# Kernel tuning notes

Hardware: AMD Instinct MI355X
Metric: run time of the kernel (lower is better)

Reference implementation:

```python
import jax, jax.numpy as jnp
import numpy as np

B, S, E, H, F, V = 4, 2048, 1024, 16, 4096, 32000
D = E // H  # head_dim = 64
LN_EPS = 1e-5


def layer_norm(x, g, b):
    mu = jnp.mean(x, axis=-1, keepdims=True)
    var = jnp.mean(jnp.square(x - mu), axis=-1, keepdims=True)
    return (x - mu) * jax.lax.rsqrt(var + LN_EPS) * g + b


def setup_inputs() -> dict:
    key = jax.random.key(0)
    ks = jax.random.split(key, 12)
    s = 0.02
    return {
        "input_ids": jax.random.randint(ks[0], (B, S), 0, V),
        "attention_mask": jnp.ones((B, S), dtype=jnp.int32),
        "emb_table": jax.random.normal(ks[1], (V, E), jnp.float32) * s,
        "Wq": jax.random.normal(ks[2], (E, E), jnp.float32) * s,
        "bq": jnp.zeros((E,), jnp.float32),
        "Wk": jax.random.normal(ks[3], (E, E), jnp.float32) * s,
        "bk": jnp.zeros((E,), jnp.float32),
        "Wv": jax.random.normal(ks[4], (E, E), jnp.float32) * s,
        "bv": jnp.zeros((E,), jnp.float32),
        "Wo": jax.random.normal(ks[5], (E, E), jnp.float32) * s,
        "bo": jnp.zeros((E,), jnp.float32),
        "ln_g": jnp.ones((E,), jnp.float32),
        "ln_b": jnp.zeros((E,), jnp.float32),
        "W1": jax.random.normal(ks[6], (E, F), jnp.float32) * s,
        "b1": jnp.zeros((F,), jnp.float32),
        "W2": jax.random.normal(ks[7], (F, E), jnp.float32) * s,
        "b2": jnp.zeros((E,), jnp.float32),
        "Wp": jax.random.normal(ks[8], (E, 3), jnp.float32) * s,
        "bp": jnp.zeros((3,), jnp.float32),
    }


def reference(input_ids, attention_mask, emb_table, Wq, bq, Wk, bk, Wv, bv,
              Wo, bo, ln_g, ln_b, W1, b1, W2, b2, Wp, bp):
    b, s = input_ids.shape
    x = emb_table[input_ids]                                  # [B,S,E]
    q = (x @ Wq + bq).reshape(b, s, H, D).transpose(0, 2, 1, 3)  # [B,H,S,D]
    k = (x @ Wk + bk).reshape(b, s, H, D).transpose(0, 2, 1, 3)
    v = (x @ Wv + bv).reshape(b, s, H, D).transpose(0, 2, 1, 3)
    scores = jnp.einsum('bhqd,bhkd->bhqk', q, k) / jnp.sqrt(jnp.float32(D))
    mask = attention_mask[:, None, None, :]                   # [B,1,1,S]
    scores = jnp.where(mask == 0, -jnp.inf, scores)
    attn = jax.nn.softmax(scores, axis=-1)
    ctx = jnp.einsum('bhqk,bhkd->bhqd', attn, v)              # [B,H,S,D]
    ctx = ctx.transpose(0, 2, 1, 3).reshape(b, s, E)
    ctx = ctx @ Wo + bo
    h = layer_norm(ctx + x, ln_g, ln_b)
    ff = jax.nn.gelu(h @ W1 + b1, approximate=False) @ W2 + b2
    logits = ff @ Wp + bp                                     # [B,S,3]
    return logits.mean(axis=1)                                # [B,3]
```

## Files before the change

kernel.cpp:

```cpp
#include <hip/hip_runtime.h>
#include <hip/hip_bf16.h>
#include <math.h>

#define BB 4
#define SS 2048
#define EE 1024
#define HH 16
#define DD 64
#define FF 4096

typedef unsigned short u16;
typedef unsigned int u32;
typedef __bf16 bf16x8 __attribute__((ext_vector_type(8)));
typedef float f32x4 __attribute__((ext_vector_type(4)));

static __device__ __forceinline__ float gelu_exact(float v){
  return 0.5f * v * (1.0f + erff(v * 0.70710678118654752f));
}

static __device__ __forceinline__ u16 f2bf(float f){
  union { float f; u32 u; } x; x.f = f;
  u32 r = x.u + 0x7FFFu + ((x.u >> 16) & 1u);
  return (u16)(r >> 16);
}
static __device__ __forceinline__ void unpack2(u32 u, float& lo, float& hi){
  union { u32 u; float f; } a, b;
  a.u = u << 16; b.u = u & 0xFFFF0000u;
  lo = a.f; hi = b.f;
}

#define GLOAD_LDS16(g, l) \
  __builtin_amdgcn_global_load_lds((const __attribute__((address_space(1))) void*)(g), \
      (__attribute__((address_space(3))) void*)(l), 16, 0, 0)

__global__ __launch_bounds__(256) void embed_kernel(const int* __restrict__ ids,
    const float* __restrict__ emb, float* __restrict__ xf, u16* __restrict__ xbf){
  int row = blockIdx.x;
  int id  = ids[row];
  float4 v = ((const float4*)(emb + (size_t)id * EE))[threadIdx.x];
  ((float4*)(xf + (size_t)row * EE))[threadIdx.x] = v;
  ushort4 u; u.x = f2bf(v.x); u.y = f2bf(v.y); u.z = f2bf(v.z); u.w = f2bf(v.w);
  ((ushort4*)(xbf + (size_t)row * EE))[threadIdx.x] = u;
}

__global__ __launch_bounds__(256) void prep_weights(const float* __restrict__ Wq,
    const float* __restrict__ Wk, const float* __restrict__ Wv,
    const float* __restrict__ Wo, const float* __restrict__ W1, u16* __restrict__ WT){
  __shared__ float tile[32][33];
  int bid = blockIdx.x;
  const float* W; u16* dst; int N, n0, k0;
  if (bid < 4096){
    W = W1; dst = WT + (size_t)4 * EE * EE; N = FF;
    n0 = (bid & 127) * 32; k0 = (bid >> 7) * 32;
  } else {
    int idx = bid - 4096;
    int which = idx >> 10, t = idx & 1023;
    W = (which == 0) ? Wq : (which == 1) ? Wk : (which == 2) ? Wv : Wo;
    dst = WT + (size_t)which * EE * EE; N = EE;
    n0 = (t & 31) * 32; k0 = (t >> 5) * 32;
  }
  int tx = threadIdx.x & 31, ty = threadIdx.x >> 5;
  #pragma unroll
  for (int i = 0; i < 4; i++)
    tile[ty + 8*i][tx] = W[(size_t)(k0 + ty + 8*i) * N + n0 + tx];
  __syncthreads();
  #pragma unroll
  for (int i = 0; i < 4; i++)
    dst[(size_t)(n0 + ty + 8*i) * EE + k0 + tx] = f2bf(tile[tx][ty + 8*i]);
}

template<int MODE>
__global__ __launch_bounds__(256) void gemm_mfma(const u16* __restrict__ A,
    const u16* __restrict__ WT, const float* __restrict__ bias,
    const float* __restrict__ biasB, const float* __restrict__ biasC,
    u16* __restrict__ C, float* __restrict__ gsum, int M, int N, int K){
  __shared__ __attribute__((aligned(16))) u16 As[128 * 32];
  __shared__ __attribute__((aligned(16))) u16 Bs[128 * 32];

  const int tid = threadIdx.x;
  const int l = tid & 63, w = tid >> 6;
  const int lm = l & 15, lq = l >> 4;
  const int wm = (w >> 1) * 64, wn = (w & 1) * 64;
  const int r0 = blockIdx.y * 128, c0 = blockIdx.x * 128;

  const int srow0 = w * 32 + (l >> 2);
  const int scol  = (l & 3) * 8;
  const u16* Ab = A  + (size_t)(r0 + srow0) * K + scol;
  const u16* Bb = WT + (size_t)(c0 + srow0) * K + scol;
  u16* AsBase0 = &As[(w * 2)     * 512];
  u16* AsBase1 = &As[(w * 2 + 1) * 512];
  u16* BsBase0 = &Bs[(w * 2)     * 512];
  u16* BsBase1 = &Bs[(w * 2 + 1) * 512];

  f32x4 acc[4][4];
  const f32x4 zero = {0.f, 0.f, 0.f, 0.f};
  #pragma unroll
  for (int mi = 0; mi < 4; mi++)
    #pragma unroll
    for (int ni = 0; ni < 4; ni++) acc[mi][ni] = zero;

  for (int k0 = 0; k0 < K; k0 += 32){
    GLOAD_LDS16(Ab + k0,                    AsBase0);
    GLOAD_LDS16(Ab + (size_t)16 * K + k0,   AsBase1);
    GLOAD_LDS16(Bb + k0,                    BsBase0);
    GLOAD_LDS16(Bb + (size_t)16 * K + k0,   BsBase1);
    __syncthreads();

    bf16x8 af[4], bf[4];
    #pragma unroll
    for (int mi = 0; mi < 4; mi++)
      af[mi] = *(const bf16x8*)&As[(wm + mi*16 + lm) * 32 + lq * 8];
    #pragma unroll
    for (int ni = 0; ni < 4; ni++)
      bf[ni] = *(const bf16x8*)&Bs[(wn + ni*16 + lm) * 32 + lq * 8];
    #pragma unroll
    for (int mi = 0; mi < 4; mi++)
      #pragma unroll
      for (int ni = 0; ni < 4; ni++)
        acc[mi][ni] = __builtin_amdgcn_mfma_f32_16x16x32_bf16(af[mi], bf[ni], acc[mi][ni], 0, 0, 0);
    __syncthreads();
  }

  if constexpr (MODE == 0){
    #pragma unroll
    for (int ni = 0; ni < 4; ni++){
      int col = c0 + wn + ni*16 + lm;
      float bcol = bias[col];
      #pragma unroll
      for (int mi = 0; mi < 4; mi++){
        #pragma unroll
        for (int r = 0; r < 4; r++){
          int row = r0 + wm + mi*16 + lq*4 + r;
          C[(size_t)row * N + col] = f2bf(acc[mi][ni][r] + bcol);
        }
      }
    }
  } else if constexpr (MODE == 2){
    #pragma unroll
    for (int ni = 0; ni < 4; ni++){
      int col3 = c0 + wn + ni*16 + lm;
      int sel  = col3 >> 10;
      int colm = col3 & 1023;
      const float* bp_ = (sel == 0) ? bias : ((sel == 1) ? biasB : biasC);
      float bcol = bp_[colm];
      u16* dst = C + (size_t)sel * ((size_t)M * N);
      #pragma unroll
      for (int mi = 0; mi < 4; mi++){
        #pragma unroll
        for (int r = 0; r < 4; r++){
          int row = r0 + wm + mi*16 + lq*4 + r;
          dst[(size_t)row * N + colm] = f2bf(acc[mi][ni][r] + bcol);
        }
      }
    }
  } else {
    const int batch = r0 >> 11;
    #pragma unroll
    for (int ni = 0; ni < 4; ni++){
      int col = c0 + wn + ni*16 + lm;
      float bcol = bias[col];
      float cs = 0.f;
      #pragma unroll
      for (int mi = 0; mi < 4; mi++)
        #pragma unroll
        for (int r = 0; r < 4; r++)
          cs += gelu_exact(acc[mi][ni][r] + bcol);
      cs += __shfl_xor(cs, 16, 64);
      cs += __shfl_xor(cs, 32, 64);
      if (lq == 0) atomicAdd(&gsum[(size_t)batch * N + col], cs);
    }
  }
}

__global__ __launch_bounds__(256, 4) void attn_mfma(const u16* __restrict__ q,
    const u16* __restrict__ k, const u16* __restrict__ v,
    const int* __restrict__ mask, u16* __restrict__ ctx){
  const int bh = blockIdx.y, b = bh >> 4, h = bh & 15;
  const int q0 = blockIdx.x * 128;
  const int tid = threadIdx.x;
  const int w = tid >> 6, l = tid & 63, lm = l & 15, lq = l >> 4;

  __shared__ __attribute__((aligned(16))) u16 Kt[64 * 72];
  __shared__ __attribute__((aligned(16))) u16 Vt[64 * 72];
  __shared__ __attribute__((aligned(16))) u16 Pw[4][32 * 72];
  __shared__ float mb[64];

  bf16x8 aq[2][2];
  #pragma unroll
  for (int mg = 0; mg < 2; mg++){
    const u16* qrow = q + (size_t)(b*SS + q0 + w*32 + mg*16 + lm) * EE + h*DD + lq*8;
    aq[mg][0] = *(const bf16x8*)qrow;
    aq[mg][1] = *(const bf16x8*)(qrow + 32);
  }

  f32x4 occ[2][4];
  const f32x4 zero = {0.f,0.f,0.f,0.f};
  #pragma unroll
  for (int mg = 0; mg < 2; mg++)
    #pragma unroll
    for (int ni = 0; ni < 4; ni++) occ[mg][ni] = zero;
  float l_part[2][4] = {{0.f,0.f,0.f,0.f},{0.f,0.f,0.f,0.f}};

  const int kkey = tid >> 2, kc16 = (tid & 3) * 16;
  const u16* kbase = k + (size_t)(b*SS + kkey) * EE + h*DD + kc16;
  const int kp = tid & 31, vd0 = (tid >> 5) * 8;
  const u16* vbase0 = v + (size_t)(b*SS + 2*kp) * EE + h*DD + vd0;
  const u16* vbase1 = vbase0 + EE;

  uint4 kr0 = *(const uint4*)(kbase);
  uint4 kr1 = *(const uint4*)(kbase + 8);
  uint4 vr0 = *(const uint4*)(vbase0);
  uint4 vr1 = *(const uint4*)(vbase1);
  float mreg = 0.f;
  if (tid < 64) mreg = (mask[b*SS + tid] != 0) ? 0.f : -1e30f;

  const float SCALE_LOG2E = 0.125f * 1.4426950408889634f;

  for (int t0 = 0; t0 < SS; t0 += 64){
    *(uint4*)&Kt[kkey*72 + kc16]     = kr0;
    *(uint4*)&Kt[kkey*72 + kc16 + 8] = kr1;
    {
      union { uint4 u; u16 s[8]; } va, vb;
      va.u = vr0; vb.u = vr1;
      #pragma unroll
      for (int i = 0; i < 8; i++){
        u32 pk = (u32)va.s[i] | ((u32)vb.s[i] << 16);
        *(u32*)&Vt[(vd0 + i)*72 + 2*kp] = pk;
      }
    }
    if (tid < 64) mb[tid] = mreg;
    __syncthreads();

    if (t0 + 64 < SS){
      kr0 = *(const uint4*)(kbase + (size_t)(t0 + 64) * EE);
      kr1 = *(const uint4*)(kbase + (size_t)(t0 + 64) * EE + 8);
      vr0 = *(const uint4*)(vbase0 + (size_t)(t0 + 64) * EE);
      vr1 = *(const uint4*)(vbase1 + (size_t)(t0 + 64) * EE);
      if (tid < 64) mreg = (mask[b*SS + t0 + 64 + tid] != 0) ? 0.f : -1e30f;
    }

    #pragma unroll
    for (int mg = 0; mg < 2; mg++){
      #pragma unroll
      for (int ni = 0; ni < 4; ni++){
        bf16x8 b0 = *(const bf16x8*)&Kt[(ni*16 + lm)*72 + lq*8];
        bf16x8 b1 = *(const bf16x8*)&Kt[(ni*16 + lm)*72 + 32 + lq*8];
        f32x4 sc = zero;
        sc = __builtin_amdgcn_mfma_f32_16x16x32_bf16(aq[mg][0], b0, sc, 0, 0, 0);
        sc = __builtin_amdgcn_mfma_f32_16x16x32_bf16(aq[mg][1], b1, sc, 0, 0, 0);
        float mbias = mb[ni*16 + lm];
        #pragma unroll
        for (int r = 0; r < 4; r++){
          float s = fminf(fmaf(sc[r], SCALE_LOG2E, mbias), 80.f);
          float p = __builtin_amdgcn_exp2f(s);
          l_part[mg][r] += p;
          Pw[w][(mg*16 + lq*4 + r)*72 + ni*16 + lm] = f2bf(p);
        }
      }
    }
    bf16x8 ap[2][2];
    #pragma unroll
    for (int mg = 0; mg < 2; mg++){
      ap[mg][0] = *(const bf16x8*)&Pw[w][(mg*16 + lm)*72 + lq*8];
      ap[mg][1] = *(const bf16x8*)&Pw[w][(mg*16 + lm)*72 + 32 + lq*8];
    }

    #pragma unroll
    for (int ni = 0; ni < 4; ni++){
      bf16x8 vb0 = *(const bf16x8*)&Vt[(ni*16 + lm)*72 + lq*8];
      bf16x8 vb1 = *(const bf16x8*)&Vt[(ni*16 + lm)*72 + 32 + lq*8];
      #pragma unroll
      for (int mg = 0; mg < 2; mg++){
        occ[mg][ni] = __builtin_amdgcn_mfma_f32_16x16x32_bf16(ap[mg][0], vb0, occ[mg][ni], 0, 0, 0);
        occ[mg][ni] = __builtin_amdgcn_mfma_f32_16x16x32_bf16(ap[mg][1], vb1, occ[mg][ni], 0, 0, 0);
      }
    }
    __syncthreads();
  }

  #pragma unroll
  for (int mg = 0; mg < 2; mg++){
    float inv[4];
    #pragma unroll
    for (int r = 0; r < 4; r++){
      float s = l_part[mg][r];
      s += __shfl_xor(s, 1, 64);
      s += __shfl_xor(s, 2, 64);
      s += __shfl_xor(s, 4, 64);
      s += __shfl_xor(s, 8, 64);
      inv[r] = 1.f / s;
    }
    #pragma unroll
    for (int ni = 0; ni < 4; ni++){
      int col = h*DD + ni*16 + lm;
      #pragma unroll
      for (int r = 0; r < 4; r++){
        int row = q0 + w*32 + mg*16 + lq*4 + r;
        ctx[(size_t)(b*SS + row) * EE + col] = f2bf(occ[mg][ni][r] * inv[r]);
      }
    }
  }
}

__global__ __launch_bounds__(256) void ln_kernel(const u16* __restrict__ c2,
    const float* __restrict__ x, const float* __restrict__ g,
    const float* __restrict__ bta, u16* __restrict__ h){
  int row = blockIdx.x, tid = threadIdx.x;
  uint2 cu = ((const uint2*)(c2 + (size_t)row * EE))[tid];
  float c0,c1,c2f,c3;
  unpack2(cu.x, c0, c1); unpack2(cu.y, c2f, c3);
  float4 xv = ((const float4*)(x + (size_t)row * EE))[tid];
  float4 y = make_float4(c0+xv.x, c1+xv.y, c2f+xv.z, c3+xv.w);
  float s  = y.x + y.y + y.z + y.w;
  float ss = y.x*y.x + y.y*y.y + y.z*y.z + y.w*y.w;
  #pragma unroll
  for (int off=32; off; off>>=1){
    s  += __shfl_xor(s,  off, 64);
    ss += __shfl_xor(ss, off, 64);
  }
  __shared__ float rs[4], rss[4];
  int w = tid >> 6;
  if ((tid & 63) == 0){ rs[w] = s; rss[w] = ss; }
  __syncthreads();
  float tot  = rs[0]+rs[1]+rs[2]+rs[3];
  float tots = rss[0]+rss[1]+rss[2]+rss[3];
  float mu  = tot  * (1.f/EE);
  float var = tots * (1.f/EE) - mu*mu;
  float inv = rsqrtf(var + 1e-5f);
  float4 gv = ((const float4*)g)[tid];
  float4 bv = ((const float4*)bta)[tid];
  ushort4 ou;
  ou.x = f2bf((y.x-mu)*inv*gv.x + bv.x);
  ou.y = f2bf((y.y-mu)*inv*gv.y + bv.y);
  ou.z = f2bf((y.z-mu)*inv*gv.z + bv.z);
  ou.w = f2bf((y.w-mu)*inv*gv.w + bv.w);
  ((ushort4*)(h + (size_t)row * EE))[tid] = ou;
}

__global__ __launch_bounds__(256) void w2wp_kernel(const float* __restrict__ W2,
    const float* __restrict__ Wp, float* __restrict__ W2Wp){
  int f0 = blockIdx.x * 8;
  int tid = threadIdx.x;
  int e0 = tid * 4;
  float wp[4][3];
  #pragma unroll
  for (int t = 0; t < 4; t++)
    #pragma unroll
    for (int j = 0; j < 3; j++) wp[t][j] = Wp[(e0 + t)*3 + j];
  __shared__ float red[3][4];
  for (int i = 0; i < 8; i++){
    int f = f0 + i;
    float4 wv = ((const float4*)(W2 + (size_t)f * EE))[tid];
    float w4[4] = {wv.x, wv.y, wv.z, wv.w};
    float p[3] = {0.f, 0.f, 0.f};
    #pragma unroll
    for (int t = 0; t < 4; t++)
      #pragma unroll
      for (int j = 0; j < 3; j++) p[j] += w4[t] * wp[t][j];
    #pragma unroll
    for (int j = 0; j < 3; j++){
      float sj = p[j];
      #pragma unroll
      for (int off = 32; off; off >>= 1) sj += __shfl_xor(sj, off, 64);
      if ((tid & 63) == 0) red[j][tid >> 6] = sj;
    }
    __syncthreads();
    if (tid < 3) W2Wp[f*3 + tid] = red[tid][0] + red[tid][1] + red[tid][2] + red[tid][3];
    __syncthreads();
  }
}

__global__ __launch_bounds__(256) void out_final(const float* __restrict__ gsum,
    const float* __restrict__ W2Wp, const float* __restrict__ b2,
    const float* __restrict__ Wp, const float* __restrict__ bp, float* __restrict__ out){
  int tid = threadIdx.x;
  float part[4][3];
  #pragma unroll
  for (int b = 0; b < 4; b++)
    #pragma unroll
    for (int j = 0; j < 3; j++) part[b][j] = 0.f;
  for (int f = tid; f < FF; f += 256){
    float w0 = W2Wp[f*3], w1 = W2Wp[f*3+1], w2v = W2Wp[f*3+2];
    #pragma unroll
    for (int b = 0; b < 4; b++){
      float g = gsum[b*FF + f] * (1.f/SS);
      part[b][0] += g * w0; part[b][1] += g * w1; part[b][2] += g * w2v;
    }
  }
  float bb[3] = {0.f, 0.f, 0.f};
  for (int e = tid; e < EE; e += 256){
    float bv = b2[e];
    bb[0] += bv * Wp[e*3]; bb[1] += bv * Wp[e*3+1]; bb[2] += bv * Wp[e*3+2];
  }
  __shared__ float red[15][4];
  int lane = tid & 63, w = tid >> 6;
  #pragma unroll
  for (int b = 0; b < 4; b++)
    #pragma unroll
    for (int j = 0; j < 3; j++){
      float s = part[b][j];
      #pragma unroll
      for (int off = 32; off; off >>= 1) s += __shfl_xor(s, off, 64);
      if (lane == 0) red[b*3 + j][w] = s;
    }
  #pragma unroll
  for (int j = 0; j < 3; j++){
    float s = bb[j];
    #pragma unroll
    for (int off = 32; off; off >>= 1) s += __shfl_xor(s, off, 64);
    if (lane == 0) red[12 + j][w] = s;
  }
  __syncthreads();
  if (tid < 12){
    int j = tid % 3;
    float s  = red[tid][0] + red[tid][1] + red[tid][2] + red[tid][3];
    float bj = red[12+j][0] + red[12+j][1] + red[12+j][2] + red[12+j][3];
    out[tid] = s + bj + bp[j];
  }
}

extern "C" void kernel_launch(void* const* d_in, const int* in_sizes, int n_in,
                              void* d_out, int out_size, void* d_ws, size_t ws_size,
                              hipStream_t stream) {
  const int M = BB * SS;
  const int* ids  = (const int*)d_in[0];
  const int* mask = (const int*)d_in[1];
  const float* emb = (const float*)d_in[2];
  const float* Wq = (const float*)d_in[3];  const float* bq = (const float*)d_in[4];
  const float* Wk = (const float*)d_in[5];  const float* bk = (const float*)d_in[6];
  const float* Wv = (const float*)d_in[7];  const float* bv = (const float*)d_in[8];
  const float* Wo = (const float*)d_in[9];  const float* bo = (const float*)d_in[10];
  const float* lg = (const float*)d_in[11]; const float* lb = (const float*)d_in[12];
  const float* W1 = (const float*)d_in[13]; const float* b1 = (const float*)d_in[14];
  const float* W2 = (const float*)d_in[15]; const float* b2 = (const float*)d_in[16];
  const float* Wp = (const float*)d_in[17]; const float* bp = (const float*)d_in[18];

  char* base = (char*)d_ws;
  const size_t SLOTF = (size_t)M * EE;
  float* xf   = (float*)base;
  u16*  xbf   = (u16*)(base + SLOTF*4);
  u16*  qbf   = (u16*)(base + SLOTF*6);
  u16*  kbf   = (u16*)(base + SLOTF*8);
  u16*  vbf   = (u16*)(base + SLOTF*10);
  u16*  ctxbf = (u16*)(base + SLOTF*12);
  u16*  c2bf  = qbf;
  u16*  hbf   = kbf;
  u16*  WqT   = (u16*)(base + SLOTF*14);
  u16*  W1T   = WqT + (size_t)4*EE*EE;
  float* gsum = (float*)(W1T + (size_t)FF*EE);
  float* w2wp = gsum + BB*FF;

  hipMemsetAsync(gsum, 0, BB*FF*sizeof(float), stream);

  embed_kernel<<<M, 256, 0, stream>>>(ids, emb, xf, xbf);

  prep_weights<<<8192, 256, 0, stream>>>(Wq, Wk, Wv, Wo, W1, WqT);
  w2wp_kernel<<<FF/8, 256, 0, stream>>>(W2, Wp, w2wp);

  gemm_mfma<2><<<dim3(3*EE/128, M/128), 256, 0, stream>>>(
      xbf, WqT, bq, bk, bv, qbf, nullptr, M, EE, EE);

  attn_mfma<<<dim3(SS/128, BB*HH), 256, 0, stream>>>(qbf, kbf, vbf, mask, ctxbf);

  gemm_mfma<0><<<dim3(EE/128, M/128), 256, 0, stream>>>(
      ctxbf, WqT + (size_t)3*EE*EE, bo, nullptr, nullptr, c2bf, nullptr, M, EE, EE);

  ln_kernel<<<M, 256, 0, stream>>>(c2bf, xf, lg, lb, hbf);

  gemm_mfma<1><<<dim3(FF/128, M/128), 256, 0, stream>>>(
      hbf, W1T, b1, nullptr, nullptr, nullptr, gsum, M, FF, EE);

  out_final<<<1, 256, 0, stream>>>(gsum, w2wp, b2, Wp, bp, (float*)d_out);
}
```

Measured before the change: 614.9 us.

## Keep attention probabilities in registers via transposed MFMA and lane shuffles

The attention kernel now computes the transposed score tile (K as the A operand, Q as B), so each lane holds probabilities laid out along the key dimension. The values are then repacked into the B-operand layout of the PV MFMA with cross-lane shuffles, which removes the per-wave shared-memory P buffer and its scalar stores and reloads. The output is likewise transposed, so row sums need only two shuffles and the context is written as 8-byte vector stores. In exchange it adds shuffle and select instructions and some register pressure, and the operand-layout changes must be exactly right to stay correct.

```diff
diff --git a/kernel.cpp b/kernel.cpp
--- a/kernel.cpp
+++ b/kernel.cpp
@@ -182,8 +182,7 @@
 
   __shared__ __attribute__((aligned(16))) u16 Kt[64 * 72];
   __shared__ __attribute__((aligned(16))) u16 Vt[64 * 72];
-  __shared__ __attribute__((aligned(16))) u16 Pw[4][32 * 72];
-  __shared__ float mb[64];
+  __shared__ __attribute__((aligned(16))) float mb[64];
 
   bf16x8 aq[2][2];
   #pragma unroll
@@ -198,8 +197,8 @@
   #pragma unroll
   for (int mg = 0; mg < 2; mg++)
     #pragma unroll
-    for (int ni = 0; ni < 4; ni++) occ[mg][ni] = zero;
-  float l_part[2][4] = {{0.f,0.f,0.f,0.f},{0.f,0.f,0.f,0.f}};
+    for (int mi = 0; mi < 4; mi++) occ[mg][mi] = zero;
+  float l_part[2] = {0.f, 0.f};
 
   const int kkey = tid >> 2, kc16 = (tid & 3) * 16;
   const u16* kbase = k + (size_t)(b*SS + kkey) * EE + h*DD + kc16;
@@ -239,40 +238,61 @@
       if (tid < 64) mreg = (mask[b*SS + t0 + 64 + tid] != 0) ? 0.f : -1e30f;
     }
 
+    bf16x8 pb[2][2];
     #pragma unroll
     for (int mg = 0; mg < 2; mg++){
-      #pragma unroll
-      for (int ni = 0; ni < 4; ni++){
-        bf16x8 b0 = *(const bf16x8*)&Kt[(ni*16 + lm)*72 + lq*8];
-        bf16x8 b1 = *(const bf16x8*)&Kt[(ni*16 + lm)*72 + 32 + lq*8];
-        f32x4 sc = zero;
-        sc = __builtin_amdgcn_mfma_f32_16x16x32_bf16(aq[mg][0], b0, sc, 0, 0, 0);
-        sc = __builtin_amdgcn_mfma_f32_16x16x32_bf16(aq[mg][1], b1, sc, 0, 0, 0);
-        float mbias = mb[ni*16 + lm];
+      float lp = 0.f;
+      #pragma unroll
+      for (int h2 = 0; h2 < 2; h2++){
+        u32 pk[2][2];
         #pragma unroll
-        for (int r = 0; r < 4; r++){
-          float s = fminf(fmaf(sc[r], SCALE_LOG2E, mbias), 80.f);
-          float p = __builtin_amdgcn_exp2f(s);
-          l_part[mg][r] += p;
-          Pw[w][(mg*16 + lq*4 + r)*72 + ni*16 + lm] = f2bf(p);
+        for (int np = 0; np < 2; np++){
+          int ni = h2*2 + np;
+          bf16x8 kf0 = *(const bf16x8*)&Kt[(ni*16 + lm)*72 + lq*8];
+          bf16x8 kf1 = *(const bf16x8*)&Kt[(ni*16 + lm)*72 + 32 + lq*8];
+          f32x4 sc = zero;
+          sc = __builtin_amdgcn_mfma_f32_16x16x32_bf16(kf0, aq[mg][0], sc, 0, 0, 0);
+          sc = __builtin_amdgcn_mfma_f32_16x16x32_bf16(kf1, aq[mg][1], sc, 0, 0, 0);
+          f32x4 mbv = *(const f32x4*)&mb[ni*16 + lq*4];
+          float p[4];
+          #pragma unroll
+          for (int r = 0; r < 4; r++){
+            float s = fminf(fmaf(sc[r], SCALE_LOG2E, mbv[r]), 80.f);
+            p[r] = __builtin_amdgcn_exp2f(s);
+            lp += p[r];
+          }
+          pk[np][0] = (u32)f2bf(p[0]) | ((u32)f2bf(p[1]) << 16);
+          pk[np][1] = (u32)f2bf(p[2]) | ((u32)f2bf(p[3]) << 16);
         }
+        int srcA = lm + 16*((2*lq)     & 3);
+        int srcB = lm + 16*((2*lq + 1) & 3);
+        u32 x0 = (u32)__shfl((int)pk[0][0], srcA, 64);
+        u32 x1 = (u32)__shfl((int)pk[0][1], srcA, 64);
+        u32 x2 = (u32)__shfl((int)pk[0][0], srcB, 64);
+        u32 x3 = (u32)__shfl((int)pk[0][1], srcB, 64);
+        u32 y0 = (u32)__shfl((int)pk[1][0], srcA, 64);
+        u32 y1 = (u32)__shfl((int)pk[1][1], srcA, 64);
+        u32 y2 = (u32)__shfl((int)pk[1][0], srcB, 64);
+        u32 y3 = (u32)__shfl((int)pk[1][1], srcB, 64);
+        bool lo = (lq < 2);
+        union { u32 u[4]; bf16x8 v; } pu;
+        pu.u[0] = lo ? x0 : y0;
+        pu.u[1] = lo ? x1 : y1;
+        pu.u[2] = lo ? x2 : y2;
+        pu.u[3] = lo ? x3 : y3;
+        pb[mg][h2] = pu.v;
       }
-    }
-    bf16x8 ap[2][2];
-    #pragma unroll
-    for (int mg = 0; mg < 2; mg++){
-      ap[mg][0] = *(const bf16x8*)&Pw[w][(mg*16 + lm)*72 + lq*8];
-      ap[mg][1] = *(const bf16x8*)&Pw[w][(mg*16 + lm)*72 + 32 + lq*8];
-    }
-
-    #pragma unroll
-    for (int ni = 0; ni < 4; ni++){
-      bf16x8 vb0 = *(const bf16x8*)&Vt[(ni*16 + lm)*72 + lq*8];
-      bf16x8 vb1 = *(const bf16x8*)&Vt[(ni*16 + lm)*72 + 32 + lq*8];
+      l_part[mg] += lp;
+    }
+
+    #pragma unroll
+    for (int mi = 0; mi < 4; mi++){
+      bf16x8 vb0 = *(const bf16x8*)&Vt[(mi*16 + lm)*72 + lq*8];
+      bf16x8 vb1 = *(const bf16x8*)&Vt[(mi*16 + lm)*72 + 32 + lq*8];
       #pragma unroll
       for (int mg = 0; mg < 2; mg++){
-        occ[mg][ni] = __builtin_amdgcn_mfma_f32_16x16x32_bf16(ap[mg][0], vb0, occ[mg][ni], 0, 0, 0);
-        occ[mg][ni] = __builtin_amdgcn_mfma_f32_16x16x32_bf16(ap[mg][1], vb1, occ[mg][ni], 0, 0, 0);
+        occ[mg][mi] = __builtin_amdgcn_mfma_f32_16x16x32_bf16(vb0, pb[mg][0], occ[mg][mi], 0, 0, 0);
+        occ[mg][mi] = __builtin_amdgcn_mfma_f32_16x16x32_bf16(vb1, pb[mg][1], occ[mg][mi], 0, 0, 0);
       }
     }
     __syncthreads();
@@ -280,24 +300,19 @@
 
   #pragma unroll
   for (int mg = 0; mg < 2; mg++){
-    float inv[4];
-    #pragma unroll
-    for (int r = 0; r < 4; r++){
-      float s = l_part[mg][r];
-      s += __shfl_xor(s, 1, 64);
-      s += __shfl_xor(s, 2, 64);
-      s += __shfl_xor(s, 4, 64);
-      s += __shfl_xor(s, 8, 64);
-      inv[r] = 1.f / s;
-    }
-    #pragma unroll
-    for (int ni = 0; ni < 4; ni++){
-      int col = h*DD + ni*16 + lm;
-      #pragma unroll
-      for (int r = 0; r < 4; r++){
-        int row = q0 + w*32 + mg*16 + lq*4 + r;
-        ctx[(size_t)(b*SS + row) * EE + col] = f2bf(occ[mg][ni][r] * inv[r]);
-      }
+    float s = l_part[mg];
+    s += __shfl_xor(s, 16, 64);
+    s += __shfl_xor(s, 32, 64);
+    float inv = 1.f / s;
+    int row = q0 + w*32 + mg*16 + lm;
+    #pragma unroll
+    for (int mi = 0; mi < 4; mi++){
+      ushort4 o;
+      o.x = f2bf(occ[mg][mi][0] * inv);
+      o.y = f2bf(occ[mg][mi][1] * inv);
+      o.z = f2bf(occ[mg][mi][2] * inv);
+      o.w = f2bf(occ[mg][mi][3] * inv);
+      *(ushort4*)&ctx[(size_t)(b*SS + row) * EE + h*DD + mi*16 + lq*4] = o;
     }
   }
 }
```

Result: slower. 652.5 us (+6.1%).
